# Kernel tuning notes

Hardware: AMD Instinct MI355X
Metric: run time of the kernel (lower is better)

The kernel has to match this reference:

```python
import jax, jax.numpy as jnp
import numpy as np

N_U, N_I, E, H = 100000, 50000, 1000000, 128


def setup_inputs() -> dict:
    key = jax.random.key(0)
    ks = jax.random.split(key, 12)
    s = 1.0 / np.sqrt(H)
    return {
        "x_user": jax.random.normal(ks[0], (N_U, H), jnp.float32),
        "x_item": jax.random.normal(ks[1], (N_I, H), jnp.float32),
        "W0": jax.random.normal(ks[2], (H, H), jnp.float32) * s,
        "b0": jnp.zeros((H,), jnp.float32),
        "W1": jax.random.normal(ks[3], (H, H), jnp.float32) * s,
        "b1": jnp.zeros((H,), jnp.float32),
        "W2": jax.random.normal(ks[4], (2 * H, H), jnp.float32) * s,
        "b2": jnp.zeros((H,), jnp.float32),
        "W3": jax.random.normal(ks[5], (2 * H, H), jnp.float32) * s,
        "b3": jnp.zeros((H,), jnp.float32),
        "Wp": jax.random.normal(ks[6], (2 * H, 2), jnp.float32) * s,
        "bp": jnp.zeros((2,), jnp.float32),
        "edge_src": jax.random.randint(ks[7], (E,), 0, N_U, jnp.int32),
        "edge_dst": jax.random.randint(ks[8], (E,), 0, N_I, jnp.int32),
    }


def _inv_sqrt_deg(idx, n):
    # DGL GraphConv: degrees clamped to min 1 before norm
    deg = jax.ops.segment_sum(jnp.ones_like(idx, jnp.float32), idx, num_segments=n)
    return jax.lax.rsqrt(jnp.maximum(deg, 1.0))


def reference(x_user, x_item, W0, b0, W1, b1, W2, b2, W3, b3, Wp, bp,
              edge_src, edge_dst):
    ones_e = None  # degrees computed from edge lists
    inv_du = _inv_sqrt_deg(edge_src, N_U)  # user degree in 'evaluate' edges
    inv_di = _inv_sqrt_deg(edge_dst, N_I)  # item degree in 'evaluate' edges

    # relation 'evaluate' (user -> item), GraphConv(h0, h0), norm='both'
    m_u = x_user * inv_du[:, None]
    agg_item = jax.ops.segment_sum(m_u[edge_src], edge_dst, num_segments=N_I)
    h_item = (agg_item * inv_di[:, None]) @ W0 + b0

    # relation 'evaluated' (item -> user, reversed edges), GraphConv(h1, h1)
    m_i = x_item * inv_di[:, None]
    agg_user = jax.ops.segment_sum(m_i[edge_dst], edge_src, num_segments=N_U)
    h_user = (agg_user * inv_du[:, None]) @ W1 + b1

    h_user = jax.nn.relu(h_user)
    h_item = jax.nn.relu(h_item)

    # concat with inputs, then per-type linear (conv2 / conv3)
    t_user = jnp.concatenate([x_user, h_user], axis=1) @ W2 + b2
    t_item = jnp.concatenate([x_item, h_item], axis=1) @ W3 + b3

    # MLPPredictor over user->item edges: gather-cat-linear
    feat_e = jnp.concatenate([t_user[edge_src], t_item[edge_dst]], axis=1)
    score = feat_e @ Wp + bp
    return jax.nn.softmax(score, axis=1)
```

## Files before the change

### kernel.cpp

```cpp
#include <hip/hip_runtime.h>
#include <hip/hip_bf16.h>


#define H 128
#define CAPC 6656

typedef __attribute__((ext_vector_type(8))) short bf16x8;
typedef __attribute__((ext_vector_type(4))) float f32x4;

__device__ __forceinline__ unsigned short f2bf(float f) {
    unsigned u = __float_as_uint(f);
    unsigned r = (u + 0x7fffu + ((u >> 16) & 1u)) >> 16;
    return (unsigned short)r;
}
__device__ __forceinline__ float bflo(unsigned b) { return __uint_as_float(b << 16); }
__device__ __forceinline__ float bfhi(unsigned b) { return __uint_as_float(b & 0xffff0000u); }
__device__ __forceinline__ float bfu(unsigned short b) { return __uint_as_float((unsigned)b << 16); }

__global__ __launch_bounds__(256) void k1_prep_pA(
    const float* __restrict__ W0, const float* __restrict__ W1,
    const float* __restrict__ W2, const float* __restrict__ b2,
    const float* __restrict__ W3, const float* __restrict__ b3,
    const float* __restrict__ Wp, const float* __restrict__ bp,
    float* __restrict__ mats,
    unsigned short* __restrict__ WswU, unsigned short* __restrict__ WswI,
    const int* __restrict__ src, const int* __restrict__ dst,
    int* __restrict__ gCurU, int* __restrict__ gCurI,
    unsigned* __restrict__ pairU, unsigned* __restrict__ pairI,
    int E, int ncu, int nci) {
    __shared__ int cntU[256], baseU[256], cntI[256], baseI[256];
    int bx = blockIdx.x, t = threadIdx.x;
    if (bx == 0) {
        int j = t >> 1, c = t & 1;
        float ax = 0.f, ah = 0.f, bx2 = 0.f, bh = 0.f;
        for (int m = 0; m < H; ++m) {
            float wpu = Wp[m * 2 + c];
            float wpi = Wp[(H + m) * 2 + c];
            ax += W2[j * H + m] * wpu;
            ah += W2[(H + j) * H + m] * wpu;
            bx2 += W3[j * H + m] * wpi;
            bh += W3[(H + j) * H + m] * wpi;
        }
        mats[      j * 2 + c] = ax;
        mats[256 + j * 2 + c] = ah;
        mats[512 + j * 2 + c] = bx2;
        mats[768 + j * 2 + c] = bh;
        if (t < 2) {
            float s1 = 0.f, s2 = 0.f;
            for (int m = 0; m < H; ++m) {
                s1 += b2[m] * Wp[m * 2 + t];
                s2 += b3[m] * Wp[(H + m) * 2 + t];
            }
            mats[1024 + t] = s1 + bp[t];
            mats[1026 + t] = s2;
        }
        return;
    }
    if (bx <= 2) {
        const float* W = (bx == 1) ? W0 : W1;
        unsigned short* o = (bx == 1) ? WswU : WswI;
        for (int i = t; i < 4096; i += 256) {
            float4 w = ((const float4*)W)[i];
            int k = i >> 5, n0 = (i & 31) * 4;
            int kb = k >> 3, kj = k & 7;
            o[(kb * 128 + n0 + 0) * 8 + kj] = f2bf(w.x);
            o[(kb * 128 + n0 + 1) * 8 + kj] = f2bf(w.y);
            o[(kb * 128 + n0 + 2) * 8 + kj] = f2bf(w.z);
            o[(kb * 128 + n0 + 3) * 8 + kj] = f2bf(w.w);
        }
        return;
    }
    int t0 = (bx - 3) * 4096;
    cntU[t] = 0; cntI[t] = 0;
    __syncthreads();
    #pragma unroll
    for (int j = 0; j < 16; ++j) {
        int e = t0 + j * 256 + t;
        if (e < E) { atomicAdd(&cntU[src[e] >> 9], 1); atomicAdd(&cntI[dst[e] >> 8], 1); }
    }
    __syncthreads();
    if (t < ncu) { int c = cntU[t]; baseU[t] = c ? (CAPC * t + atomicAdd(&gCurU[t], c)) : 0; }
    if (t < nci) { int c = cntI[t]; baseI[t] = c ? (CAPC * t + atomicAdd(&gCurI[t], c)) : 0; }
    __syncthreads();
    #pragma unroll
    for (int j = 0; j < 16; ++j) {
        int e = t0 + j * 256 + t;
        if (e < E) {
            int s = src[e], d = dst[e];
            int bu = s >> 9, bi = d >> 8;
            int r1 = atomicSub(&cntU[bu], 1) - 1;
            int i1 = baseU[bu] + r1;
            if (i1 < CAPC * (bu + 1))
                pairU[i1] = ((unsigned)(s & 511) << 20) | (unsigned)d;
            int r2 = atomicSub(&cntI[bi], 1) - 1;
            int i2 = baseI[bi] + r2;
            if (i2 < CAPC * (bi + 1))
                pairI[i2] = ((unsigned)(d & 255) << 20) | (unsigned)s;
        }
    }
}

__global__ __launch_bounds__(256) void k2_build_mfma(
    const unsigned* __restrict__ pairU, const unsigned* __restrict__ pairI,
    const int* __restrict__ gCurU, const int* __restrict__ gCurI,
    int2* __restrict__ offU, int2* __restrict__ offI,
    float* __restrict__ invU, float* __restrict__ invI,
    int* __restrict__ valU, int* __restrict__ valI,
    const float* __restrict__ xU, const float* __restrict__ xI,
    const unsigned short* __restrict__ WswU, const unsigned short* __restrict__ WswI,
    unsigned short* __restrict__ yU, unsigned short* __restrict__ yI,
    const float* __restrict__ mats,
    float2* __restrict__ gxU, float2* __restrict__ gxI,
    int NU, int NI, int ncu, int nci, int NBU, int NBI) {
    __shared__ __align__(16) char SMEM[34816];
    int nPB = ncu + nci;
    int t = threadIdx.x;

    if (blockIdx.x < (unsigned)nPB) {
        bool us = blockIdx.x < (unsigned)ncu;
        int cb = us ? blockIdx.x : blockIdx.x - ncu;
        const unsigned* pairs = us ? pairU : pairI;
        int size = us ? gCurU[cb] : gCurI[cb];
        if (size > CAPC) size = CAPC;
        int start = cb * CAPC;
        int nodesPer = us ? 512 : 256;
        int nodeBase = cb * nodesPer;
        int n = us ? NU : NI;
        int2* off = us ? offU : offI;
        float* inv = us ? invU : invI;
        int* val = us ? valU : valI;

        int* cnt  = (int*)SMEM;
        int* pref = cnt + nodesPer;
        int* part = pref + nodesPer;
        int* stage = part + 256;

        for (int i = t; i < nodesPer; i += 256) cnt[i] = 0;
        __syncthreads();
        for (int i = t; i < size; i += 256) atomicAdd(&cnt[pairs[start + i] >> 20], 1);
        __syncthreads();
        int g = nodesPer >> 8;
        int b0 = t * g;
        int lv0 = cnt[b0], lv1 = (g == 2) ? cnt[b0 + 1] : 0;
        int lsum = lv0 + lv1;
        part[t] = lsum; __syncthreads();
        for (int o2 = 1; o2 < 256; o2 <<= 1) {
            int v = (t >= o2) ? part[t - o2] : 0; __syncthreads();
            part[t] += v; __syncthreads();
        }
        int excl = part[t] - lsum;
        pref[b0] = excl;
        if (g == 2) pref[b0 + 1] = excl + lv0;
        __syncthreads();
        for (int i = t; i < nodesPer; i += 256) {
            int node = nodeBase + i;
            if (node < n) {
                int st = pref[i];
                off[node] = make_int2(start + st, start + st + cnt[i]);
                inv[node] = rsqrtf(fmaxf((float)cnt[i], 1.0f));
            }
        }
        __syncthreads();
        for (int i = t; i < size; i += 256) {
            unsigned p = pairs[start + i];
            int r = atomicAdd(&pref[p >> 20], 1);
            stage[r] = (int)(p & 0xFFFFFu);
        }
        __syncthreads();
        for (int i = t; i < size; i += 256) val[start + i] = stage[i];
        return;
    }

    unsigned short* As = (unsigned short*)SMEM;
    int mb = blockIdx.x - nPB;
    bool us = mb < NBU;
    int tile = us ? mb : mb - NBU;
    const float* x = us ? xU : xI;
    const unsigned short* Wsw = us ? WswU : WswI;
    unsigned short* y = us ? yU : yI;
    const float* Mx = mats + (us ? 0 : 512);
    const float* cv = mats + (us ? 1024 : 1026);
    float2* gx = us ? gxU : gxI;
    int n = us ? NU : NI;
    int row0 = tile << 7;

    for (int it = 0; it < 16; ++it) {
        int i = it * 256 + t;
        int m = i >> 5, c4 = i & 31;
        int row = row0 + m;
        float4 v = (row < n) ? ((const float4*)x)[(size_t)row * 32 + c4]
                             : make_float4(0.f, 0.f, 0.f, 0.f);
        int k0 = c4 * 4;
        ushort4 s4; s4.x = f2bf(v.x); s4.y = f2bf(v.y); s4.z = f2bf(v.z); s4.w = f2bf(v.w);
        *(ushort4*)&As[((k0 >> 3) * 128 + m) * 8 + (k0 & 7)] = s4;
    }
    __syncthreads();

    int w = t >> 6, l = t & 63;
    int lane15 = l & 15, quad = l >> 4;

    f32x4 acc[2][8];
    #pragma unroll
    for (int rt = 0; rt < 2; ++rt)
        #pragma unroll
        for (int c = 0; c < 8; ++c) acc[rt][c] = (f32x4){0.f, 0.f, 0.f, 0.f};

    #pragma unroll
    for (int ks = 0; ks < 4; ++ks) {
        int kb = ks * 4 + quad;
        bf16x8 a0 = *(const bf16x8*)&As[(kb * 128 + w * 32 + lane15) * 8];
        bf16x8 a1 = *(const bf16x8*)&As[(kb * 128 + w * 32 + 16 + lane15) * 8];
        #pragma unroll
        for (int c = 0; c < 8; ++c) {
            bf16x8 b = *(const bf16x8*)&Wsw[(size_t)(kb * 128 + c * 16 + lane15) * 8];
            acc[0][c] = __builtin_amdgcn_mfma_f32_16x16x32_bf16(a0, b, acc[0][c], 0, 0, 0);
            acc[1][c] = __builtin_amdgcn_mfma_f32_16x16x32_bf16(a1, b, acc[1][c], 0, 0, 0);
        }
    }

    {
        int row = t >> 1, cc = t & 1;
        float p = 0.f;
        for (int kb = 0; kb < 16; ++kb) {
            const unsigned short* ap = &As[(kb * 128 + row) * 8];
            #pragma unroll
            for (int j = 0; j < 8; ++j)
                p += bfu(ap[j]) * Mx[(kb * 8 + j) * 2 + cc];
        }
        int grow = row0 + row;
        if (grow < n) ((float*)&gx[grow])[cc] = p + cv[cc];
    }
    __syncthreads();

    const int LSTR = 136;
    unsigned short* SMu = (unsigned short*)SMEM;
    unsigned short* Lw = SMu + w * 32 * LSTR;
    #pragma unroll
    for (int rt = 0; rt < 2; ++rt) {
        #pragma unroll
        for (int r = 0; r < 4; ++r) {
            int lrow = rt * 16 + quad * 4 + r;
            #pragma unroll
            for (int c = 0; c < 8; ++c)
                Lw[lrow * LSTR + c * 16 + lane15] = f2bf(acc[rt][c][r]);
        }
    }
    #pragma unroll
    for (int pass = 0; pass < 8; ++pass) {
        int lrow = pass * 4 + quad;
        int grow = row0 + w * 32 + lrow;
        uint4 v = *(uint4*)&Lw[lrow * LSTR + lane15 * 8];
        if (grow < n) *(uint4*)&y[(size_t)grow * 128 + lane15 * 8] = v;
    }
}

__global__ __launch_bounds__(256) void gather_kernel(
    const int2* __restrict__ offU, const int* __restrict__ valU,
    const int2* __restrict__ offI, const int* __restrict__ valI,
    const unsigned short* __restrict__ yU, const unsigned short* __restrict__ yI,
    const float* __restrict__ invU, const float* __restrict__ invI,
    const float* __restrict__ b0, const float* __restrict__ b1,
    const float* __restrict__ mats,
    const float2* __restrict__ gxU, const float2* __restrict__ gxI,
    float2* __restrict__ su, float2* __restrict__ si,
    int NU, int NI, int GU) {
    bool us = blockIdx.x < (unsigned)GU;
    int nb = us ? blockIdx.x : blockIdx.x - GU;
    const int2* off = us ? offU : offI;
    const int* val = us ? valU : valI;
    const unsigned short* yo = us ? yI : yU;
    const float* invo = us ? invI : invU;
    const float* inv = us ? invU : invI;
    const float* bv = us ? b1 : b0;
    const float* Mh = mats + (us ? 256 : 768);
    const float2* gx = us ? gxU : gxI;
    float2* so = us ? su : si;
    int n = us ? NU : NI;

    int g = threadIdx.x >> 4, t = threadIdx.x & 15, j0 = t * 8;
    int u = nb * 16 + g;
    if (u >= n) return;

    float a0 = 0, a1 = 0, a2 = 0, a3 = 0, a4 = 0, a5 = 0, a6 = 0, a7 = 0;
    int2 oe = off[u];
    int k = oe.x, end = oe.y;
    for (; k + 4 <= end; k += 4) {
        int v0 = val[k], v1 = val[k + 1], v2 = val[k + 2], v3 = val[k + 3];
        float i0 = invo[v0], i1 = invo[v1], i2 = invo[v2], i3 = invo[v3];
        uint4 w0 = *(const uint4*)(yo + (size_t)v0 * H + j0);
        uint4 w1 = *(const uint4*)(yo + (size_t)v1 * H + j0);
        uint4 w2 = *(const uint4*)(yo + (size_t)v2 * H + j0);
        uint4 w3 = *(const uint4*)(yo + (size_t)v3 * H + j0);
        a0 += bflo(w0.x) * i0 + bflo(w1.x) * i1 + bflo(w2.x) * i2 + bflo(w3.x) * i3;
        a1 += bfhi(w0.x) * i0 + bfhi(w1.x) * i1 + bfhi(w2.x) * i2 + bfhi(w3.x) * i3;
        a2 += bflo(w0.y) * i0 + bflo(w1.y) * i1 + bflo(w2.y) * i2 + bflo(w3.y) * i3;
        a3 += bfhi(w0.y) * i0 + bfhi(w1.y) * i1 + bfhi(w2.y) * i2 + bfhi(w3.y) * i3;
        a4 += bflo(w0.z) * i0 + bflo(w1.z) * i1 + bflo(w2.z) * i2 + bflo(w3.z) * i3;
        a5 += bfhi(w0.z) * i0 + bfhi(w1.z) * i1 + bfhi(w2.z) * i2 + bfhi(w3.z) * i3;
        a6 += bflo(w0.w) * i0 + bflo(w1.w) * i1 + bflo(w2.w) * i2 + bflo(w3.w) * i3;
        a7 += bfhi(w0.w) * i0 + bfhi(w1.w) * i1 + bfhi(w2.w) * i2 + bfhi(w3.w) * i3;
    }
    for (; k < end; ++k) {
        int v0 = val[k];
        float i0 = invo[v0];
        uint4 w0 = *(const uint4*)(yo + (size_t)v0 * H + j0);
        a0 += bflo(w0.x) * i0; a1 += bfhi(w0.x) * i0;
        a2 += bflo(w0.y) * i0; a3 += bfhi(w0.y) * i0;
        a4 += bflo(w0.z) * i0; a5 += bfhi(w0.z) * i0;
        a6 += bflo(w0.w) * i0; a7 += bfhi(w0.w) * i0;
    }
    float iv = inv[u];
    float4 bb0 = *(const float4*)(bv + j0), bb1 = *(const float4*)(bv + j0 + 4);
    float h0 = fmaxf(a0 * iv + bb0.x, 0.f), h1 = fmaxf(a1 * iv + bb0.y, 0.f);
    float h2 = fmaxf(a2 * iv + bb0.z, 0.f), h3 = fmaxf(a3 * iv + bb0.w, 0.f);
    float h4 = fmaxf(a4 * iv + bb1.x, 0.f), h5 = fmaxf(a5 * iv + bb1.y, 0.f);
    float h6 = fmaxf(a6 * iv + bb1.z, 0.f), h7 = fmaxf(a7 * iv + bb1.w, 0.f);
    float4 m0 = *(const float4*)(Mh + j0 * 2),      m1 = *(const float4*)(Mh + j0 * 2 + 4);
    float4 m2 = *(const float4*)(Mh + j0 * 2 + 8),  m3 = *(const float4*)(Mh + j0 * 2 + 12);
    float p0 = h0 * m0.x + h1 * m0.z + h2 * m1.x + h3 * m1.z
             + h4 * m2.x + h5 * m2.z + h6 * m3.x + h7 * m3.z;
    float p1 = h0 * m0.y + h1 * m0.w + h2 * m1.y + h3 * m1.w
             + h4 * m2.y + h5 * m2.w + h6 * m3.y + h7 * m3.w;
    #pragma unroll
    for (int o = 1; o < 16; o <<= 1) { p0 += __shfl_xor(p0, o); p1 += __shfl_xor(p1, o); }
    if (t == 0) {
        float2 gg = gx[u];
        so[u] = make_float2(p0 + gg.x, p1 + gg.y);
    }
}

__global__ void edge_kernel(const int* __restrict__ src, const int* __restrict__ dst,
                            const float2* __restrict__ su, const float2* __restrict__ si,
                            float2* __restrict__ out, int E) {
    int e0 = (blockIdx.x * 256 + threadIdx.x) * 2;
    if (e0 >= E) return;
    int2 s2 = *(const int2*)(src + e0);
    int2 d2 = *(const int2*)(dst + e0);
    float2 a = su[s2.x], b = si[d2.x];
    float l0 = a.x + b.x, l1 = a.y + b.y;
    float m = fmaxf(l0, l1);
    float q0 = __expf(l0 - m), q1 = __expf(l1 - m);
    float r = 1.0f / (q0 + q1);
    out[e0] = make_float2(q0 * r, q1 * r);
    if (e0 + 1 < E) {
        a = su[s2.y]; b = si[d2.y];
        l0 = a.x + b.x; l1 = a.y + b.y;
        m = fmaxf(l0, l1);
        q0 = __expf(l0 - m); q1 = __expf(l1 - m);
        r = 1.0f / (q0 + q1);
        out[e0 + 1] = make_float2(q0 * r, q1 * r);
    }
}

extern "C" void kernel_launch(void* const* d_in, const int* in_sizes, int n_in,
                              void* d_out, int out_size, void* d_ws, size_t ws_size,
                              hipStream_t stream) {
    const float* x_user = (const float*)d_in[0];
    const float* x_item = (const float*)d_in[1];
    const float* W0 = (const float*)d_in[2];
    const float* b0 = (const float*)d_in[3];
    const float* W1 = (const float*)d_in[4];
    const float* b1 = (const float*)d_in[5];
    const float* W2 = (const float*)d_in[6];
    const float* b2 = (const float*)d_in[7];
    const float* W3 = (const float*)d_in[8];
    const float* b3 = (const float*)d_in[9];
    const float* Wp = (const float*)d_in[10];
    const float* bp = (const float*)d_in[11];
    const int* esrc = (const int*)d_in[12];
    const int* edst = (const int*)d_in[13];

    const int NU = in_sizes[0] / H;
    const int NI = in_sizes[1] / H;
    const int E  = in_sizes[12];
    const int NCU = (NU + 511) >> 9;
    const int NCI = (NI + 255) >> 8;
    const int NBU = (NU + 127) >> 7;
    const int NBI = (NI + 127) >> 7;
    const int GU = (NU + 15) >> 4, GI = (NI + 15) >> 4;

    auto rnd = [](size_t x) { return (x + 63) & ~(size_t)63; };
    char* base = (char*)d_ws;
    size_t o = 0;
    auto alloc = [&](size_t elems) { void* p = base + o * 4; o += rnd(elems); return p; };

    float* inv_du = (float*)alloc(NU);
    float* inv_di = (float*)alloc(NI);
    float2* su    = (float2*)alloc((size_t)NU * 2);
    float2* si    = (float2*)alloc((size_t)NI * 2);
    float2* gxU   = (float2*)alloc((size_t)NU * 2);
    float2* gxI   = (float2*)alloc((size_t)NI * 2);
    float* mats   = (float*)alloc(1056);
    size_t cur_off = o;
    int* gCurU = (int*)alloc(NCU);
    int* gCurI = (int*)alloc(NCI);
    size_t cur_words = o - cur_off;
    int2* offU = (int2*)alloc((size_t)NU * 2);
    int2* offI = (int2*)alloc((size_t)NI * 2);
    int* valU  = (int*)alloc((size_t)NCU * CAPC);
    int* valI  = (int*)alloc((size_t)NCI * CAPC);
    unsigned* pairU = (unsigned*)alloc((size_t)NCU * CAPC);
    unsigned* pairI = (unsigned*)alloc((size_t)NCI * CAPC);
    unsigned short* WswU = (unsigned short*)alloc(8192);
    unsigned short* WswI = (unsigned short*)alloc(8192);
    unsigned short* yU = (unsigned short*)alloc((size_t)NU * 64);
    unsigned short* yI = (unsigned short*)alloc((size_t)NI * 64);

    hipMemsetAsync(gCurU, 0, cur_words * 4, stream);

    int pa_blocks = (E + 4095) / 4096;
    k1_prep_pA<<<3 + pa_blocks, 256, 0, stream>>>(
        W0, W1, W2, b2, W3, b3, Wp, bp, mats, WswU, WswI,
        esrc, edst, gCurU, gCurI, pairU, pairI, E, NCU, NCI);

    k2_build_mfma<<<NCU + NCI + NBU + NBI, 256, 0, stream>>>(
        pairU, pairI, gCurU, gCurI, offU, offI, inv_du, inv_di, valU, valI,
        x_user, x_item, WswU, WswI, yU, yI, mats, gxU, gxI,
        NU, NI, NCU, NCI, NBU, NBI);

    gather_kernel<<<GU + GI, 256, 0, stream>>>(
        offU, valU, offI, valI, yU, yI, inv_du, inv_di, b0, b1, mats,
        gxU, gxI, su, si, NU, NI, GU);

    edge_kernel<<<(E / 2 + 255) / 256, 256, 0, stream>>>(esrc, edst, su, si, (float2*)d_out, E);
}
```

Baseline: 283.3 us.

## Regroup kernel schedule: co-launch edge partition with MFMA transform, split pass B

Moves the edge-bucketing pass A out of the prep kernel and co-launches it with the MFMA feature-transform blocks. Pass B (CSR build) becomes its own kernel, and the counter memset is replaced by zeroing inside the prep kernel. The goal is to overlap the atomic-heavy partitioning with the GEMM work and drop one memset launch. It also switches gather index loads and edge output stores to nontemporal accesses to reduce cache pollution. Kernel count stays the same, but the dependency structure changes, and pass B now waits on the GEMM blocks finishing.

```diff
diff --git a/kernel.cpp b/kernel.cpp
--- a/kernel.cpp
+++ b/kernel.cpp
@@ -7,6 +7,7 @@
 
 typedef __attribute__((ext_vector_type(8))) short bf16x8;
 typedef __attribute__((ext_vector_type(4))) float f32x4;
+typedef __attribute__((ext_vector_type(2))) float f32x2;
 
 __device__ __forceinline__ unsigned short f2bf(float f) {
     unsigned u = __float_as_uint(f);
@@ -17,18 +18,14 @@
 __device__ __forceinline__ float bfhi(unsigned b) { return __uint_as_float(b & 0xffff0000u); }
 __device__ __forceinline__ float bfu(unsigned short b) { return __uint_as_float((unsigned)b << 16); }
 
-__global__ __launch_bounds__(256) void k1_prep_pA(
+__global__ __launch_bounds__(256) void k0_prep(
     const float* __restrict__ W0, const float* __restrict__ W1,
     const float* __restrict__ W2, const float* __restrict__ b2,
     const float* __restrict__ W3, const float* __restrict__ b3,
     const float* __restrict__ Wp, const float* __restrict__ bp,
     float* __restrict__ mats,
     unsigned short* __restrict__ WswU, unsigned short* __restrict__ WswI,
-    const int* __restrict__ src, const int* __restrict__ dst,
-    int* __restrict__ gCurU, int* __restrict__ gCurI,
-    unsigned* __restrict__ pairU, unsigned* __restrict__ pairI,
-    int E, int ncu, int nci) {
-    __shared__ int cntU[256], baseU[256], cntI[256], baseI[256];
+    int* __restrict__ gCur, int curWords) {
     int bx = blockIdx.x, t = threadIdx.x;
     if (bx == 0) {
         int j = t >> 1, c = t & 1;
@@ -70,109 +67,60 @@
         }
         return;
     }
-    int t0 = (bx - 3) * 4096;
-    cntU[t] = 0; cntI[t] = 0;
-    __syncthreads();
-    #pragma unroll
-    for (int j = 0; j < 16; ++j) {
-        int e = t0 + j * 256 + t;
-        if (e < E) { atomicAdd(&cntU[src[e] >> 9], 1); atomicAdd(&cntI[dst[e] >> 8], 1); }
-    }
-    __syncthreads();
-    if (t < ncu) { int c = cntU[t]; baseU[t] = c ? (CAPC * t + atomicAdd(&gCurU[t], c)) : 0; }
-    if (t < nci) { int c = cntI[t]; baseI[t] = c ? (CAPC * t + atomicAdd(&gCurI[t], c)) : 0; }
-    __syncthreads();
-    #pragma unroll
-    for (int j = 0; j < 16; ++j) {
-        int e = t0 + j * 256 + t;
-        if (e < E) {
-            int s = src[e], d = dst[e];
-            int bu = s >> 9, bi = d >> 8;
-            int r1 = atomicSub(&cntU[bu], 1) - 1;
-            int i1 = baseU[bu] + r1;
-            if (i1 < CAPC * (bu + 1))
-                pairU[i1] = ((unsigned)(s & 511) << 20) | (unsigned)d;
-            int r2 = atomicSub(&cntI[bi], 1) - 1;
-            int i2 = baseI[bi] + r2;
-            if (i2 < CAPC * (bi + 1))
-                pairI[i2] = ((unsigned)(d & 255) << 20) | (unsigned)s;
-        }
-    }
-}
-
-__global__ __launch_bounds__(256) void k2_build_mfma(
-    const unsigned* __restrict__ pairU, const unsigned* __restrict__ pairI,
-    const int* __restrict__ gCurU, const int* __restrict__ gCurI,
-    int2* __restrict__ offU, int2* __restrict__ offI,
-    float* __restrict__ invU, float* __restrict__ invI,
-    int* __restrict__ valU, int* __restrict__ valI,
+    for (int i = t; i < curWords; i += 256) gCur[i] = 0;
+}
+
+__global__ __launch_bounds__(256) void k1_pA_mfma(
+    const int* __restrict__ src, const int* __restrict__ dst,
+    int* __restrict__ gCurU, int* __restrict__ gCurI,
+    unsigned* __restrict__ pairU, unsigned* __restrict__ pairI,
     const float* __restrict__ xU, const float* __restrict__ xI,
     const unsigned short* __restrict__ WswU, const unsigned short* __restrict__ WswI,
     unsigned short* __restrict__ yU, unsigned short* __restrict__ yI,
     const float* __restrict__ mats,
     float2* __restrict__ gxU, float2* __restrict__ gxI,
-    int NU, int NI, int ncu, int nci, int NBU, int NBI) {
+    int E, int ncu, int nci, int NU, int NI, int PA, int NBU) {
     __shared__ __align__(16) char SMEM[34816];
-    int nPB = ncu + nci;
     int t = threadIdx.x;
 
-    if (blockIdx.x < (unsigned)nPB) {
-        bool us = blockIdx.x < (unsigned)ncu;
-        int cb = us ? blockIdx.x : blockIdx.x - ncu;
-        const unsigned* pairs = us ? pairU : pairI;
-        int size = us ? gCurU[cb] : gCurI[cb];
-        if (size > CAPC) size = CAPC;
-        int start = cb * CAPC;
-        int nodesPer = us ? 512 : 256;
-        int nodeBase = cb * nodesPer;
-        int n = us ? NU : NI;
-        int2* off = us ? offU : offI;
-        float* inv = us ? invU : invI;
-        int* val = us ? valU : valI;
-
-        int* cnt  = (int*)SMEM;
-        int* pref = cnt + nodesPer;
-        int* part = pref + nodesPer;
-        int* stage = part + 256;
-
-        for (int i = t; i < nodesPer; i += 256) cnt[i] = 0;
+    if (blockIdx.x < (unsigned)PA) {
+        int* cntU  = (int*)SMEM;
+        int* baseU = cntU + 256;
+        int* cntI  = baseU + 256;
+        int* baseI = cntI + 256;
+        int t0 = blockIdx.x * 4096;
+        cntU[t] = 0; cntI[t] = 0;
         __syncthreads();
-        for (int i = t; i < size; i += 256) atomicAdd(&cnt[pairs[start + i] >> 20], 1);
+        #pragma unroll
+        for (int j = 0; j < 16; ++j) {
+            int e = t0 + j * 256 + t;
+            if (e < E) { atomicAdd(&cntU[src[e] >> 9], 1); atomicAdd(&cntI[dst[e] >> 8], 1); }
+        }
         __syncthreads();
-        int g = nodesPer >> 8;
-        int b0 = t * g;
-        int lv0 = cnt[b0], lv1 = (g == 2) ? cnt[b0 + 1] : 0;
-        int lsum = lv0 + lv1;
-        part[t] = lsum; __syncthreads();
-        for (int o2 = 1; o2 < 256; o2 <<= 1) {
-            int v = (t >= o2) ? part[t - o2] : 0; __syncthreads();
-            part[t] += v; __syncthreads();
-        }
-        int excl = part[t] - lsum;
-        pref[b0] = excl;
-        if (g == 2) pref[b0 + 1] = excl + lv0;
+        if (t < ncu) { int c = cntU[t]; baseU[t] = c ? (CAPC * t + atomicAdd(&gCurU[t], c)) : 0; }
+        if (t < nci) { int c = cntI[t]; baseI[t] = c ? (CAPC * t + atomicAdd(&gCurI[t], c)) : 0; }
         __syncthreads();
-        for (int i = t; i < nodesPer; i += 256) {
-            int node = nodeBase + i;
-            if (node < n) {
-                int st = pref[i];
-                off[node] = make_int2(start + st, start + st + cnt[i]);
-                inv[node] = rsqrtf(fmaxf((float)cnt[i], 1.0f));
+        #pragma unroll
+        for (int j = 0; j < 16; ++j) {
+            int e = t0 + j * 256 + t;
+            if (e < E) {
+                int s = src[e], d = dst[e];
+                int bu = s >> 9, bi = d >> 8;
+                int r1 = atomicSub(&cntU[bu], 1) - 1;
+                int i1 = baseU[bu] + r1;
+                if (i1 < CAPC * (bu + 1))
+                    pairU[i1] = ((unsigned)(s & 511) << 20) | (unsigned)d;
+                int r2 = atomicSub(&cntI[bi], 1) - 1;
+                int i2 = baseI[bi] + r2;
+                if (i2 < CAPC * (bi + 1))
+                    pairI[i2] = ((unsigned)(d & 255) << 20) | (unsigned)s;
             }
         }
-        __syncthreads();
-        for (int i = t; i < size; i += 256) {
-            unsigned p = pairs[start + i];
-            int r = atomicAdd(&pref[p >> 20], 1);
-            stage[r] = (int)(p & 0xFFFFFu);
-        }
-        __syncthreads();
-        for (int i = t; i < size; i += 256) val[start + i] = stage[i];
         return;
     }
 
     unsigned short* As = (unsigned short*)SMEM;
-    int mb = blockIdx.x - nPB;
+    int mb = blockIdx.x - PA;
     bool us = mb < NBU;
     int tile = us ? mb : mb - NBU;
     const float* x = us ? xU : xI;
@@ -252,6 +200,68 @@
         uint4 v = *(uint4*)&Lw[lrow * LSTR + lane15 * 8];
         if (grow < n) *(uint4*)&y[(size_t)grow * 128 + lane15 * 8] = v;
     }
+}
+
+__global__ __launch_bounds__(256) void k2_passB(
+    const unsigned* __restrict__ pairU, const unsigned* __restrict__ pairI,
+    const int* __restrict__ gCurU, const int* __restrict__ gCurI,
+    int2* __restrict__ offU, int2* __restrict__ offI,
+    float* __restrict__ invU, float* __restrict__ invI,
+    int* __restrict__ valU, int* __restrict__ valI,
+    int NU, int NI, int ncu) {
+    __shared__ __align__(16) char SMEM[34816];
+    int t = threadIdx.x;
+    bool us = blockIdx.x < (unsigned)ncu;
+    int cb = us ? blockIdx.x : blockIdx.x - ncu;
+    const unsigned* pairs = us ? pairU : pairI;
+    int size = us ? gCurU[cb] : gCurI[cb];
+    if (size > CAPC) size = CAPC;
+    int start = cb * CAPC;
+    int nodesPer = us ? 512 : 256;
+    int nodeBase = cb * nodesPer;
+    int n = us ? NU : NI;
+    int2* off = us ? offU : offI;
+    float* inv = us ? invU : invI;
+    int* val = us ? valU : valI;
+
+    int* cnt  = (int*)SMEM;
+    int* pref = cnt + nodesPer;
+    int* part = pref + nodesPer;
+    int* stage = part + 256;
+
+    for (int i = t; i < nodesPer; i += 256) cnt[i] = 0;
+    __syncthreads();
+    for (int i = t; i < size; i += 256) atomicAdd(&cnt[pairs[start + i] >> 20], 1);
+    __syncthreads();
+    int g = nodesPer >> 8;
+    int b0 = t * g;
+    int lv0 = cnt[b0], lv1 = (g == 2) ? cnt[b0 + 1] : 0;
+    int lsum = lv0 + lv1;
+    part[t] = lsum; __syncthreads();
+    for (int o2 = 1; o2 < 256; o2 <<= 1) {
+        int v = (t >= o2) ? part[t - o2] : 0; __syncthreads();
+        part[t] += v; __syncthreads();
+    }
+    int excl = part[t] - lsum;
+    pref[b0] = excl;
+    if (g == 2) pref[b0 + 1] = excl + lv0;
+    __syncthreads();
+    for (int i = t; i < nodesPer; i += 256) {
+        int node = nodeBase + i;
+        if (node < n) {
+            int st = pref[i];
+            off[node] = make_int2(start + st, start + st + cnt[i]);
+            inv[node] = rsqrtf(fmaxf((float)cnt[i], 1.0f));
+        }
+    }
+    __syncthreads();
+    for (int i = t; i < size; i += 256) {
+        unsigned p = pairs[start + i];
+        int r = atomicAdd(&pref[p >> 20], 1);
+        stage[r] = (int)(p & 0xFFFFFu);
+    }
+    __syncthreads();
+    for (int i = t; i < size; i += 256) val[start + i] = stage[i];
 }
 
 __global__ __launch_bounds__(256) void gather_kernel(
@@ -285,7 +295,10 @@
     int2 oe = off[u];
     int k = oe.x, end = oe.y;
     for (; k + 4 <= end; k += 4) {
-        int v0 = val[k], v1 = val[k + 1], v2 = val[k + 2], v3 = val[k + 3];
+        int v0 = __builtin_nontemporal_load(val + k);
+        int v1 = __builtin_nontemporal_load(val + k + 1);
+        int v2 = __builtin_nontemporal_load(val + k + 2);
+        int v3 = __builtin_nontemporal_load(val + k + 3);
         float i0 = invo[v0], i1 = invo[v1], i2 = invo[v2], i3 = invo[v3];
         uint4 w0 = *(const uint4*)(yo + (size_t)v0 * H + j0);
         uint4 w1 = *(const uint4*)(yo + (size_t)v1 * H + j0);
@@ -301,7 +314,7 @@
         a7 += bfhi(w0.w) * i0 + bfhi(w1.w) * i1 + bfhi(w2.w) * i2 + bfhi(w3.w) * i3;
     }
     for (; k < end; ++k) {
-        int v0 = val[k];
+        int v0 = __builtin_nontemporal_load(val + k);
         float i0 = invo[v0];
         uint4 w0 = *(const uint4*)(yo + (size_t)v0 * H + j0);
         a0 += bflo(w0.x) * i0; a1 += bfhi(w0.x) * i0;
@@ -331,7 +344,7 @@
 
 __global__ void edge_kernel(const int* __restrict__ src, const int* __restrict__ dst,
                             const float2* __restrict__ su, const float2* __restrict__ si,
-                            float2* __restrict__ out, int E) {
+                            float* __restrict__ out, int E) {
     int e0 = (blockIdx.x * 256 + threadIdx.x) * 2;
     if (e0 >= E) return;
     int2 s2 = *(const int2*)(src + e0);
@@ -341,14 +354,14 @@
     float m = fmaxf(l0, l1);
     float q0 = __expf(l0 - m), q1 = __expf(l1 - m);
     float r = 1.0f / (q0 + q1);
-    out[e0] = make_float2(q0 * r, q1 * r);
+    __builtin_nontemporal_store((f32x2){q0 * r, q1 * r}, (f32x2*)(out + (size_t)e0 * 2));
     if (e0 + 1 < E) {
         a = su[s2.y]; b = si[d2.y];
         l0 = a.x + b.x; l1 = a.y + b.y;
         m = fmaxf(l0, l1);
         q0 = __expf(l0 - m); q1 = __expf(l1 - m);
         r = 1.0f / (q0 + q1);
-        out[e0 + 1] = make_float2(q0 * r, q1 * r);
+        __builtin_nontemporal_store((f32x2){q0 * r, q1 * r}, (f32x2*)(out + (size_t)(e0 + 1) * 2));
     }
 }
 
@@ -406,21 +419,22 @@
     unsigned short* yU = (unsigned short*)alloc((size_t)NU * 64);
     unsigned short* yI = (unsigned short*)alloc((size_t)NI * 64);
 
-    hipMemsetAsync(gCurU, 0, cur_words * 4, stream);
-
-    int pa_blocks = (E + 4095) / 4096;
-    k1_prep_pA<<<3 + pa_blocks, 256, 0, stream>>>(
-        W0, W1, W2, b2, W3, b3, Wp, bp, mats, WswU, WswI,
-        esrc, edst, gCurU, gCurI, pairU, pairI, E, NCU, NCI);
-
-    k2_build_mfma<<<NCU + NCI + NBU + NBI, 256, 0, stream>>>(
+    k0_prep<<<4, 256, 0, stream>>>(
+        W0, W1, W2, b2, W3, b3, Wp, bp, mats, WswU, WswI, gCurU, (int)cur_words);
+
+    int PA = (E + 4095) / 4096;
+    k1_pA_mfma<<<PA + NBU + NBI, 256, 0, stream>>>(
+        esrc, edst, gCurU, gCurI, pairU, pairI,
+        x_user, x_item, WswU, WswI, yU, yI, mats, gxU, gxI,
+        E, NCU, NCI, NU, NI, PA, NBU);
+
+    k2_passB<<<NCU + NCI, 256, 0, stream>>>(
         pairU, pairI, gCurU, gCurI, offU, offI, inv_du, inv_di, valU, valI,
-        x_user, x_item, WswU, WswI, yU, yI, mats, gxU, gxI,
-        NU, NI, NCU, NCI, NBU, NBI);
+        NU, NI, NCU);
 
     gather_kernel<<<GU + GI, 256, 0, stream>>>(
         offU, valU, offI, valI, yU, yI, inv_du, inv_di, b0, b1, mats,
         gxU, gxI, su, si, NU, NI, GU);
 
-    edge_kernel<<<(E / 2 + 255) / 256, 256, 0, stream>>>(esrc, edst, su, si, (float2*)d_out, E);
-}
+    edge_kernel<<<(E / 2 + 255) / 256, 256, 0, stream>>>(esrc, edst, su, si, (float*)d_out, E);
+}
```

Result: slower. 308.4 us (+8.9%).
